# Kernel optimization log

Hardware: AMD Instinct MI355X
Metric: run time of the kernel (lower is better)

The kernel has to match this reference:

```python
import jax, jax.numpy as jnp
import numpy as np

MARGIN = 0.2
LAMBDA_CLS = 1.0
LAMBDA_TRIPLET = 1.0
EPS = 1e-6  # matches torch pairwise_distance eps inside TripletMarginLoss
B, D, C = 8192, 192, 1024


def setup_inputs() -> dict:
    key = jax.random.key(0)
    k1, k2, k3 = jax.random.split(key, 3)
    embeddings = jax.random.normal(k1, (B, D), dtype=jnp.float32)
    logits = jax.random.normal(k2, (B, C), dtype=jnp.float32)
    targets = jax.random.randint(k3, (B,), 0, C, dtype=jnp.int64)
    return {"embeddings": embeddings, "logits": logits, "targets": targets}


def reference(embeddings, logits, targets):
    # ---- classification loss: mean cross entropy ----
    logp = jax.nn.log_softmax(logits, axis=-1)
    cls_loss = -jnp.mean(jnp.take_along_axis(logp, targets[:, None], axis=1))

    # ---- vectorized hard triplet mining (mining='hard'), on detached embeddings ----
    e = jax.lax.stop_gradient(embeddings)
    sq = jnp.sum(e * e, axis=1)                       # [B]
    d2 = sq[:, None] + sq[None, :] - 2.0 * (e @ e.T)  # [B, B]
    dist = jnp.sqrt(jnp.maximum(d2, 0.0))

    same = targets[:, None] == targets[None, :]       # [B, B]
    eye = jnp.eye(targets.shape[0], dtype=bool)
    pos_mask = same & ~eye
    neg_mask = ~same
    valid = pos_mask.any(axis=1) & neg_mask.any(axis=1)

    # hard positive: farthest same-speaker; hard negative: closest other-speaker
    pos_idx = jnp.argmax(jnp.where(pos_mask, dist, -jnp.inf), axis=1)
    neg_idx = jnp.argmin(jnp.where(neg_mask, dist, jnp.inf), axis=1)

    # ---- triplet margin loss on live embeddings ----
    a = embeddings
    p = embeddings[pos_idx]
    n = embeddings[neg_idx]
    d_ap = jnp.linalg.norm(a - p + EPS, axis=1)
    d_an = jnp.linalg.norm(a - n + EPS, axis=1)
    per_triplet = jnp.maximum(d_ap - d_an + MARGIN, 0.0)

    w = valid.astype(per_triplet.dtype)
    cnt = jnp.sum(w)
    trip_loss = jnp.where(cnt > 0, jnp.sum(per_triplet * w) / jnp.maximum(cnt, 1.0), 0.0)

    return LAMBDA_CLS * cls_loss + LAMBDA_TRIPLET * trip_loss
```

## Files before the change

### kernel.cpp

```cpp
#include <hip/hip_runtime.h>
#include <math.h>

#define B_N    8192
#define D_DIM  192
#define C_CLS  1024
#define MARGIN 0.2f
#define EPS_T  1e-6f

#define TI     128
#define TJ     128
#define JSPLIT 8
#define JLEN   (B_N / JSPLIT)
#define NT     (JLEN / TJ)
#define RB     512

typedef short v8s  __attribute__((ext_vector_type(8)));
typedef float v16f __attribute__((ext_vector_type(16)));

typedef __attribute__((address_space(3))) unsigned int       lds_u32;
typedef __attribute__((address_space(1))) const unsigned int glb_u32;

__device__ __forceinline__ void gll16(const void* g, void* l) {
  __builtin_amdgcn_global_load_lds((glb_u32*)g, (lds_u32*)l, 16, 0, 0);
}

__device__ __forceinline__ int swz(int r, int s) {
  return r * RB + ((s ^ (r & 31)) << 4);
}

__device__ __forceinline__ void stage_tile(char* dst, const char* src, int tid) {
  #pragma unroll
  for (int k = 0; k < 16; ++k) {
    int c = k * 256 + tid;
    int r = c >> 5;
    int s = (c & 31) ^ (r & 31);
    int so = (s < 24) ? (s << 4) : 0;
    gll16(src + r * 384 + so, dst + (k * 256 + (tid & ~63)) * 16);
  }
}

__device__ __forceinline__ unsigned fkey(float f) {
  unsigned u = __float_as_uint(f);
  return (u & 0x80000000u) ? ~u : (u | 0x80000000u);
}

__device__ __forceinline__ unsigned short to_bf(float x) {
  unsigned u = __float_as_uint(x);
  u += 0x7fffu + ((u >> 16) & 1u);
  return (unsigned short)(u >> 16);
}

__global__ __launch_bounds__(256) void prep_kernel(
    const float* __restrict__ e, unsigned short* __restrict__ ebf,
    float* __restrict__ sq,
    unsigned long long* __restrict__ posw, unsigned long long* __restrict__ negw,
    float* __restrict__ accum) {
  int w = threadIdx.x >> 6, lane = threadIdx.x & 63;
  int row = blockIdx.x * 4 + w;
  const float* p = e + (size_t)row * D_DIM;
  float v0 = p[lane], v1 = p[lane + 64], v2 = p[lane + 128];
  unsigned short* q = ebf + (size_t)row * D_DIM;
  q[lane] = to_bf(v0); q[lane + 64] = to_bf(v1); q[lane + 128] = to_bf(v2);
  float s = v0 * v0 + v1 * v1 + v2 * v2;
  #pragma unroll
  for (int off = 32; off; off >>= 1) s += __shfl_xor(s, off);
  if (lane == 0) sq[row] = s;
  int b = blockIdx.x;
  if (b < 32)       posw[b * 256 + threadIdx.x] = 0ULL;
  else if (b < 64)  negw[(b - 32) * 256 + threadIdx.x] = ~0ULL;
  else if (b == 64 && threadIdx.x < 4) ((unsigned*)accum)[threadIdx.x] = 0u;
}

__global__ __launch_bounds__(256, 2) void mine_kernel(
    const unsigned short* __restrict__ ebf, const int* __restrict__ tgt,
    const float* __restrict__ sq, const float* __restrict__ logits,
    unsigned long long* __restrict__ posw, unsigned long long* __restrict__ negw,
    float* __restrict__ accum) {
  __shared__ unsigned short lds_b[TJ * (RB / 2)];
  __shared__ float lds_sq[JLEN];
  __shared__ int   lds_tg[JLEN];
  __shared__ float ce_part[4];

  const int tid  = threadIdx.x;
  const int w    = tid >> 6;
  const int lane = tid & 63;
  const int n5   = lane & 31;
  const int h    = lane >> 5;
  const int wj   = w & 1;
  const int wi   = w >> 1;
  const int i0 = blockIdx.x * TI;
  const int jb = blockIdx.y * JLEN;

  char* ldsc = (char*)lds_b;

  stage_tile(ldsc, (const char*)(ebf + (size_t)i0 * D_DIM), tid);
  gll16((const char*)(sq  + jb) + tid * 16, (char*)lds_sq + (tid & ~63) * 16);
  gll16((const char*)(tgt + jb) + tid * 16, (char*)lds_tg + (tid & ~63) * 16);

  int my_t[2];
  #pragma unroll
  for (int tb = 0; tb < 2; ++tb) my_t[tb] = tgt[i0 + wi * 64 + tb * 32 + n5];

  __syncthreads();

  v8s bfrag[2][12];
  #pragma unroll
  for (int tb = 0; tb < 2; ++tb)
    #pragma unroll
    for (int kc = 0; kc < 12; ++kc)
      bfrag[tb][kc] = *(const v8s*)(ldsc + swz(wi * 64 + tb * 32 + n5, 2 * kc + h));

  float    pv[2] = {-3.4e38f, -3.4e38f}, nv[2] = {3.4e38f, 3.4e38f};
  unsigned pi_[2] = {0u, 0u}, ni_[2] = {0xFFFFFFFFu, 0xFFFFFFFFu};

  for (int t = 0; t < NT; ++t) {
    __syncthreads();
    stage_tile(ldsc, (const char*)(ebf + (size_t)(jb + t * TJ) * D_DIM), tid);
    __syncthreads();

    v16f acc[2][2];
    #pragma unroll
    for (int ta = 0; ta < 2; ++ta)
      #pragma unroll
      for (int tb = 0; tb < 2; ++tb)
        #pragma unroll
        for (int r = 0; r < 16; ++r) acc[ta][tb][r] = 0.f;

    #pragma unroll
    for (int kc = 0; kc < 12; ++kc) {
      v8s afr0 = *(const v8s*)(ldsc + swz(wj * 64 +  0 + n5, 2 * kc + h));
      v8s afr1 = *(const v8s*)(ldsc + swz(wj * 64 + 32 + n5, 2 * kc + h));
      acc[0][0] = __builtin_amdgcn_mfma_f32_32x32x16_bf16(afr0, bfrag[0][kc], acc[0][0], 0, 0, 0);
      acc[0][1] = __builtin_amdgcn_mfma_f32_32x32x16_bf16(afr0, bfrag[1][kc], acc[0][1], 0, 0, 0);
      acc[1][0] = __builtin_amdgcn_mfma_f32_32x32x16_bf16(afr1, bfrag[0][kc], acc[1][0], 0, 0, 0);
      acc[1][1] = __builtin_amdgcn_mfma_f32_32x32x16_bf16(afr1, bfrag[1][kc], acc[1][1], 0, 0, 0);
    }

    const int j0 = jb + t * TJ;
    const int jt = t * TJ;
    #pragma unroll
    for (int ta = 0; ta < 2; ++ta)
      #pragma unroll
      for (int p = 0; p < 4; ++p) {
        int jb4 = wj * 64 + ta * 32 + p * 8 + h * 4;
        float4 s4 = *(const float4*)&lds_sq[jt + jb4];
        int4   t4 = *(const int4*)&lds_tg[jt + jb4];
        #pragma unroll
        for (int q = 0; q < 4; ++q) {
          float sv = (q == 0) ? s4.x : (q == 1) ? s4.y : (q == 2) ? s4.z : s4.w;
          int   tv = (q == 0) ? t4.x : (q == 1) ? t4.y : (q == 2) ? t4.z : t4.w;
          unsigned jg = (unsigned)(j0 + jb4 + q);
          #pragma unroll
          for (int tb = 0; tb < 2; ++tb) {
            float val = fmaf(acc[ta][tb][p * 4 + q], -2.0f, sv);
            bool same = (tv == my_t[tb]);
            if (same  && val > pv[tb]) { pv[tb] = val; pi_[tb] = jg; }
            if (!same && val < nv[tb]) { nv[tb] = val; ni_[tb] = jg; }
          }
        }
      }
  }

  #pragma unroll
  for (int tb = 0; tb < 2; ++tb) {
    unsigned long long pk =
        ((unsigned long long)fkey(pv[tb]) << 32) | (unsigned long long)(unsigned)(~pi_[tb]);
    unsigned long long nk =
        ((unsigned long long)fkey(nv[tb]) << 32) | (unsigned long long)ni_[tb];
    unsigned long long po = __shfl_xor(pk, 32);
    unsigned long long no = __shfl_xor(nk, 32);
    pk = pk > po ? pk : po;
    nk = nk < no ? nk : no;
    if (h == 0) {
      int irow = i0 + wi * 64 + tb * 32 + n5;
      atomicMax(&posw[irow], pk);
      atomicMin(&negw[irow], nk);
    }
  }

  {
    int blin = blockIdx.y * 64 + blockIdx.x;
    float ce_acc = 0.f;
    #pragma unroll
    for (int it = 0; it < 4; ++it) {
      int row = blin * 16 + it * 4 + w;
      const float* lp = logits + (size_t)row * C_CLS;
      float4 x[4];
      #pragma unroll
      for (int u = 0; u < 4; ++u) x[u] = *(const float4*)(lp + lane * 4 + 256 * u);
      float m = -3.4e38f;
      #pragma unroll
      for (int u = 0; u < 4; ++u)
        m = fmaxf(m, fmaxf(fmaxf(x[u].x, x[u].y), fmaxf(x[u].z, x[u].w)));
      #pragma unroll
      for (int off = 32; off; off >>= 1) m = fmaxf(m, __shfl_xor(m, off));
      float s = 0.f;
      #pragma unroll
      for (int u = 0; u < 4; ++u)
        s += __expf(x[u].x - m) + __expf(x[u].y - m) +
             __expf(x[u].z - m) + __expf(x[u].w - m);
      #pragma unroll
      for (int off = 32; off; off >>= 1) s += __shfl_xor(s, off);
      if (lane == 0) ce_acc += m + __logf(s) - lp[tgt[row]];
    }
    if (lane == 0) ce_part[w] = ce_acc;
  }
  __syncthreads();
  if (tid == 0)
    atomicAdd(&accum[0], ce_part[0] + ce_part[1] + ce_part[2] + ce_part[3]);
}

__global__ __launch_bounds__(1024) void trip_fin_kernel(
    const float* __restrict__ e,
    const unsigned long long* __restrict__ posw,
    const unsigned long long* __restrict__ negw,
    float* __restrict__ accum, float* __restrict__ out) {
  __shared__ float ssum[16];
  __shared__ float scnt[16];
  int w = threadIdx.x >> 6, lane = threadIdx.x & 63;
  int i = blockIdx.x * 16 + w;
  unsigned long long pp = posw[i], np = negw[i];
  unsigned pidx = ~(unsigned)pp;
  unsigned nidx = (unsigned)np;
  float res = 0.f, c = 0.f;
  if (pp != 0ULL && np != ~0ULL && pidx != (unsigned)i) {
    const float* pa = e + (size_t)i * D_DIM;
    const float* pb = e + (size_t)pidx * D_DIM;
    const float* pc = e + (size_t)nidx * D_DIM;
    float dap = 0.f, dan = 0.f;
    #pragma unroll
    for (int t = 0; t < 3; ++t) {
      int k = lane + 64 * t;
      float av = pa[k];
      float d1 = av - pb[k] + EPS_T;
      float d2 = av - pc[k] + EPS_T;
      dap += d1 * d1;
      dan += d2 * d2;
    }
    #pragma unroll
    for (int off = 32; off; off >>= 1) {
      dap += __shfl_xor(dap, off);
      dan += __shfl_xor(dan, off);
    }
    res = fmaxf(sqrtf(dap) - sqrtf(dan) + MARGIN, 0.f);
    c = 1.f;
  }
  if (lane == 0) { ssum[w] = res; scnt[w] = c; }
  __syncthreads();
  if (threadIdx.x == 0) {
    float a = 0.f, b = 0.f;
    #pragma unroll
    for (int k = 0; k < 16; ++k) { a += ssum[k]; b += scnt[k]; }
    atomicAdd(&accum[1], a);
    atomicAdd(&accum[2], b);
    __threadfence();
    unsigned old = atomicAdd((unsigned*)&accum[3], 1u);
    if (old == 511u) {
      __threadfence();
      float cls = atomicAdd(&accum[0], 0.f);
      float ts  = atomicAdd(&accum[1], 0.f);
      float tc  = atomicAdd(&accum[2], 0.f);
      float trip = (tc > 0.f) ? ts / fmaxf(tc, 1.f) : 0.f;
      out[0] = cls / (float)B_N + trip;
    }
  }
}

extern "C" void kernel_launch(void* const* d_in, const int* in_sizes, int n_in,
                              void* d_out, int out_size, void* d_ws, size_t ws_size,
                              hipStream_t stream) {
  const float* emb    = (const float*)d_in[0];
  const float* logits = (const float*)d_in[1];
  const int*   tgt    = (const int*)d_in[2];
  float* out = (float*)d_out;

  char* ws = (char*)d_ws;
  unsigned short* ebf = (unsigned short*)ws;
  unsigned long long* posw = (unsigned long long*)(ws + 3145728);
  unsigned long long* negw = (unsigned long long*)(ws + 3145728 + 65536);
  float* sq    = (float*)(ws + 3145728 + 131072);
  float* accum = (float*)(ws + 3145728 + 163840);

  prep_kernel<<<2048, 256, 0, stream>>>(emb, ebf, sq, posw, negw, accum);
  mine_kernel<<<dim3(B_N / TI, JSPLIT), 256, 0, stream>>>(ebf, tgt, sq, logits, posw, negw, accum);
  trip_fin_kernel<<<512, 1024, 0, stream>>>(emb, posw, negw, accum, out);
}
```

Before: 157.1 us.

## Read MFMA fragments directly from global memory and fuse triplet finalize into mining

Drops the LDS staging of the j-tile and its two barriers per iteration, so each wave loads its A fragments straight from the bf16 embedding buffer in global memory (relying on L2/L1 reuse). The separate triplet/finalize kernel is removed: the last of the JSPLIT blocks for each row block, detected with a per-row-block completion counter, computes the triplet losses for its 128 rows and performs the final reduction. This saves a kernel launch and the LDS traffic, but it risks uncoalesced global loads with less reuse and adds a serialized tail of work in the last blocks.

```diff
diff --git a/kernel.cpp b/kernel.cpp
--- a/kernel.cpp
+++ b/kernel.cpp
@@ -12,32 +12,10 @@
 #define JSPLIT 8
 #define JLEN   (B_N / JSPLIT)
 #define NT     (JLEN / TJ)
-#define RB     512
+#define RBY    384
 
 typedef short v8s  __attribute__((ext_vector_type(8)));
 typedef float v16f __attribute__((ext_vector_type(16)));
-
-typedef __attribute__((address_space(3))) unsigned int       lds_u32;
-typedef __attribute__((address_space(1))) const unsigned int glb_u32;
-
-__device__ __forceinline__ void gll16(const void* g, void* l) {
-  __builtin_amdgcn_global_load_lds((glb_u32*)g, (lds_u32*)l, 16, 0, 0);
-}
-
-__device__ __forceinline__ int swz(int r, int s) {
-  return r * RB + ((s ^ (r & 31)) << 4);
-}
-
-__device__ __forceinline__ void stage_tile(char* dst, const char* src, int tid) {
-  #pragma unroll
-  for (int k = 0; k < 16; ++k) {
-    int c = k * 256 + tid;
-    int r = c >> 5;
-    int s = (c & 31) ^ (r & 31);
-    int so = (s < 24) ? (s << 4) : 0;
-    gll16(src + r * 384 + so, dst + (k * 256 + (tid & ~63)) * 16);
-  }
-}
 
 __device__ __forceinline__ unsigned fkey(float f) {
   unsigned u = __float_as_uint(f);
@@ -54,7 +32,7 @@
     const float* __restrict__ e, unsigned short* __restrict__ ebf,
     float* __restrict__ sq,
     unsigned long long* __restrict__ posw, unsigned long long* __restrict__ negw,
-    float* __restrict__ accum) {
+    float* __restrict__ accum, unsigned* __restrict__ donecnt) {
   int w = threadIdx.x >> 6, lane = threadIdx.x & 63;
   int row = blockIdx.x * 4 + w;
   const float* p = e + (size_t)row * D_DIM;
@@ -69,17 +47,21 @@
   if (b < 32)       posw[b * 256 + threadIdx.x] = 0ULL;
   else if (b < 64)  negw[(b - 32) * 256 + threadIdx.x] = ~0ULL;
   else if (b == 64 && threadIdx.x < 4) ((unsigned*)accum)[threadIdx.x] = 0u;
+  else if (b == 65 && threadIdx.x < 64) donecnt[threadIdx.x] = 0u;
 }
 
 __global__ __launch_bounds__(256, 2) void mine_kernel(
     const unsigned short* __restrict__ ebf, const int* __restrict__ tgt,
     const float* __restrict__ sq, const float* __restrict__ logits,
+    const float* __restrict__ emb,
     unsigned long long* __restrict__ posw, unsigned long long* __restrict__ negw,
-    float* __restrict__ accum) {
-  __shared__ unsigned short lds_b[TJ * (RB / 2)];
+    float* __restrict__ accum, unsigned* __restrict__ donecnt,
+    float* __restrict__ out) {
   __shared__ float lds_sq[JLEN];
   __shared__ int   lds_tg[JLEN];
   __shared__ float ce_part[4];
+  __shared__ float red[8];
+  __shared__ unsigned sdone;
 
   const int tid  = threadIdx.x;
   const int w    = tid >> 6;
@@ -91,32 +73,32 @@
   const int i0 = blockIdx.x * TI;
   const int jb = blockIdx.y * JLEN;
 
-  char* ldsc = (char*)lds_b;
-
-  stage_tile(ldsc, (const char*)(ebf + (size_t)i0 * D_DIM), tid);
-  gll16((const char*)(sq  + jb) + tid * 16, (char*)lds_sq + (tid & ~63) * 16);
-  gll16((const char*)(tgt + jb) + tid * 16, (char*)lds_tg + (tid & ~63) * 16);
-
-  int my_t[2];
-  #pragma unroll
-  for (int tb = 0; tb < 2; ++tb) my_t[tb] = tgt[i0 + wi * 64 + tb * 32 + n5];
-
-  __syncthreads();
-
+  *(float4*)&lds_sq[tid * 4] = *(const float4*)(sq  + jb + tid * 4);
+  *(int4*)  &lds_tg[tid * 4] = *(const int4*)  (tgt + jb + tid * 4);
+
+  const char* eb = (const char*)ebf;
   v8s bfrag[2][12];
   #pragma unroll
-  for (int tb = 0; tb < 2; ++tb)
+  for (int tb = 0; tb < 2; ++tb) {
+    const char* bp = eb + (size_t)(i0 + wi * 64 + tb * 32 + n5) * RBY + h * 16;
     #pragma unroll
     for (int kc = 0; kc < 12; ++kc)
-      bfrag[tb][kc] = *(const v8s*)(ldsc + swz(wi * 64 + tb * 32 + n5, 2 * kc + h));
+      bfrag[tb][kc] = *(const v8s*)(bp + kc * 32);
+  }
+  int my_t[2];
+  my_t[0] = tgt[i0 + wi * 64 + n5];
+  my_t[1] = tgt[i0 + wi * 64 + 32 + n5];
+
+  __syncthreads();
 
   float    pv[2] = {-3.4e38f, -3.4e38f}, nv[2] = {3.4e38f, 3.4e38f};
   unsigned pi_[2] = {0u, 0u}, ni_[2] = {0xFFFFFFFFu, 0xFFFFFFFFu};
 
+  #pragma unroll 1
   for (int t = 0; t < NT; ++t) {
-    __syncthreads();
-    stage_tile(ldsc, (const char*)(ebf + (size_t)(jb + t * TJ) * D_DIM), tid);
-    __syncthreads();
+    const int j0 = jb + t * TJ;
+    const char* ar0 = eb + (size_t)(j0 + wj * 64 +  0 + n5) * RBY + h * 16;
+    const char* ar1 = eb + (size_t)(j0 + wj * 64 + 32 + n5) * RBY + h * 16;
 
     v16f acc[2][2];
     #pragma unroll
@@ -128,15 +110,14 @@
 
     #pragma unroll
     for (int kc = 0; kc < 12; ++kc) {
-      v8s afr0 = *(const v8s*)(ldsc + swz(wj * 64 +  0 + n5, 2 * kc + h));
-      v8s afr1 = *(const v8s*)(ldsc + swz(wj * 64 + 32 + n5, 2 * kc + h));
+      v8s afr0 = *(const v8s*)(ar0 + kc * 32);
+      v8s afr1 = *(const v8s*)(ar1 + kc * 32);
       acc[0][0] = __builtin_amdgcn_mfma_f32_32x32x16_bf16(afr0, bfrag[0][kc], acc[0][0], 0, 0, 0);
       acc[0][1] = __builtin_amdgcn_mfma_f32_32x32x16_bf16(afr0, bfrag[1][kc], acc[0][1], 0, 0, 0);
       acc[1][0] = __builtin_amdgcn_mfma_f32_32x32x16_bf16(afr1, bfrag[0][kc], acc[1][0], 0, 0, 0);
       acc[1][1] = __builtin_amdgcn_mfma_f32_32x32x16_bf16(afr1, bfrag[1][kc], acc[1][1], 0, 0, 0);
     }
 
-    const int j0 = jb + t * TJ;
     const int jt = t * TJ;
     #pragma unroll
     for (int ta = 0; ta < 2; ++ta)
@@ -149,7 +130,7 @@
         for (int q = 0; q < 4; ++q) {
           float sv = (q == 0) ? s4.x : (q == 1) ? s4.y : (q == 2) ? s4.z : s4.w;
           int   tv = (q == 0) ? t4.x : (q == 1) ? t4.y : (q == 2) ? t4.z : t4.w;
-          unsigned jg = (unsigned)(j0 + jb4 + q);
+          unsigned jg = (unsigned)(jb + jt + jb4 + q);
           #pragma unroll
           for (int tb = 0; tb < 2; ++tb) {
             float val = fmaf(acc[ta][tb][p * 4 + q], -2.0f, sv);
@@ -208,60 +189,65 @@
   __syncthreads();
   if (tid == 0)
     atomicAdd(&accum[0], ce_part[0] + ce_part[1] + ce_part[2] + ce_part[3]);
-}
-
-__global__ __launch_bounds__(1024) void trip_fin_kernel(
-    const float* __restrict__ e,
-    const unsigned long long* __restrict__ posw,
-    const unsigned long long* __restrict__ negw,
-    float* __restrict__ accum, float* __restrict__ out) {
-  __shared__ float ssum[16];
-  __shared__ float scnt[16];
-  int w = threadIdx.x >> 6, lane = threadIdx.x & 63;
-  int i = blockIdx.x * 16 + w;
-  unsigned long long pp = posw[i], np = negw[i];
-  unsigned pidx = ~(unsigned)pp;
-  unsigned nidx = (unsigned)np;
-  float res = 0.f, c = 0.f;
-  if (pp != 0ULL && np != ~0ULL && pidx != (unsigned)i) {
-    const float* pa = e + (size_t)i * D_DIM;
-    const float* pb = e + (size_t)pidx * D_DIM;
-    const float* pc = e + (size_t)nidx * D_DIM;
-    float dap = 0.f, dan = 0.f;
-    #pragma unroll
-    for (int t = 0; t < 3; ++t) {
-      int k = lane + 64 * t;
-      float av = pa[k];
-      float d1 = av - pb[k] + EPS_T;
-      float d2 = av - pc[k] + EPS_T;
-      dap += d1 * d1;
-      dan += d2 * d2;
-    }
-    #pragma unroll
-    for (int off = 32; off; off >>= 1) {
-      dap += __shfl_xor(dap, off);
-      dan += __shfl_xor(dan, off);
-    }
-    res = fmaxf(sqrtf(dap) - sqrtf(dan) + MARGIN, 0.f);
-    c = 1.f;
-  }
-  if (lane == 0) { ssum[w] = res; scnt[w] = c; }
+  __threadfence();
+
+  if (tid == 0) sdone = atomicAdd(&donecnt[blockIdx.x], 1u);
   __syncthreads();
-  if (threadIdx.x == 0) {
-    float a = 0.f, b = 0.f;
-    #pragma unroll
-    for (int k = 0; k < 16; ++k) { a += ssum[k]; b += scnt[k]; }
-    atomicAdd(&accum[1], a);
-    atomicAdd(&accum[2], b);
-    __threadfence();
-    unsigned old = atomicAdd((unsigned*)&accum[3], 1u);
-    if (old == 511u) {
+  if (sdone == (unsigned)(JSPLIT - 1)) {
+    float lsum = 0.f, lcnt = 0.f;
+    #pragma unroll 1
+    for (int r = w; r < TI; r += 4) {
+      int i = i0 + r;
+      unsigned long long pp = 0ULL, np = 0ULL;
+      if (lane == 0) {
+        pp = atomicOr(&posw[i], 0ULL);
+        np = atomicOr(&negw[i], 0ULL);
+      }
+      pp = __shfl(pp, 0); np = __shfl(np, 0);
+      unsigned pidx = ~(unsigned)pp;
+      unsigned nidx = (unsigned)np;
+      float res = 0.f, c = 0.f;
+      if (pp != 0ULL && np != ~0ULL && pidx != (unsigned)i) {
+        const float* pa = emb + (size_t)i * D_DIM;
+        const float* pb = emb + (size_t)pidx * D_DIM;
+        const float* pc = emb + (size_t)nidx * D_DIM;
+        float dap = 0.f, dan = 0.f;
+        #pragma unroll
+        for (int u = 0; u < 3; ++u) {
+          int k = lane + 64 * u;
+          float av = pa[k];
+          float d1 = av - pb[k] + EPS_T;
+          float d2 = av - pc[k] + EPS_T;
+          dap += d1 * d1;
+          dan += d2 * d2;
+        }
+        #pragma unroll
+        for (int off = 32; off; off >>= 1) {
+          dap += __shfl_xor(dap, off);
+          dan += __shfl_xor(dan, off);
+        }
+        res = fmaxf(sqrtf(dap) - sqrtf(dan) + MARGIN, 0.f);
+        c = 1.f;
+      }
+      if (lane == 0) { lsum += res; lcnt += c; }
+    }
+    if (lane == 0) { red[w] = lsum; red[4 + w] = lcnt; }
+    __syncthreads();
+    if (tid == 0) {
+      float a = red[0] + red[1] + red[2] + red[3];
+      float b = red[4] + red[5] + red[6] + red[7];
+      atomicAdd(&accum[1], a);
+      atomicAdd(&accum[2], b);
       __threadfence();
-      float cls = atomicAdd(&accum[0], 0.f);
-      float ts  = atomicAdd(&accum[1], 0.f);
-      float tc  = atomicAdd(&accum[2], 0.f);
-      float trip = (tc > 0.f) ? ts / fmaxf(tc, 1.f) : 0.f;
-      out[0] = cls / (float)B_N + trip;
+      unsigned old = atomicAdd((unsigned*)&accum[3], 1u);
+      if (old == 63u) {
+        __threadfence();
+        float cls = atomicAdd(&accum[0], 0.f);
+        float ts  = atomicAdd(&accum[1], 0.f);
+        float tc  = atomicAdd(&accum[2], 0.f);
+        float trip = (tc > 0.f) ? ts / fmaxf(tc, 1.f) : 0.f;
+        out[0] = cls / (float)B_N + trip;
+      }
     }
   }
 }
@@ -280,8 +266,9 @@
   unsigned long long* negw = (unsigned long long*)(ws + 3145728 + 65536);
   float* sq    = (float*)(ws + 3145728 + 131072);
   float* accum = (float*)(ws + 3145728 + 163840);
-
-  prep_kernel<<<2048, 256, 0, stream>>>(emb, ebf, sq, posw, negw, accum);
-  mine_kernel<<<dim3(B_N / TI, JSPLIT), 256, 0, stream>>>(ebf, tgt, sq, logits, posw, negw, accum);
-  trip_fin_kernel<<<512, 1024, 0, stream>>>(emb, posw, negw, accum, out);
-}
+  unsigned* donecnt = (unsigned*)(ws + 3145728 + 163856);
+
+  prep_kernel<<<2048, 256, 0, stream>>>(emb, ebf, sq, posw, negw, accum, donecnt);
+  mine_kernel<<<dim3(B_N / TI, JSPLIT), 256, 0, stream>>>(
+      ebf, tgt, sq, logits, emb, posw, negw, accum, donecnt, out);
+}
```

Measured after the change: 225.7 us. 43.7% more time.
